# Optimization experiments

Measured on AMD Instinct MI355X. Metric: run time of the kernel, lower is better.

Reference implementation:

```python
import jax, jax.numpy as jnp
import numpy as np

B = 8192          # batch_size
NB = 4096         # num_banks (== mask length)
PAD = NB // 2     # reflect pad on each side


def setup_inputs() -> dict:
    key = jax.random.key(0)
    k1, k2, k3 = jax.random.split(key, 3)
    logits = jax.random.normal(k1, (NB,), dtype=jnp.float32) * 0.1
    u = jax.random.uniform(k2, (B, NB), dtype=jnp.float32)          # Bernoulli uniforms
    shift = jax.random.randint(k3, (B,), 0, NB, dtype=jnp.int32)    # per-sample shift
    return {"logits": logits, "u": u, "shift": shift}


def reference(logits, u, shift):
    # Bernoulli(sigmoid(logits)) sample via inverse-CDF on externally supplied uniforms
    p = jax.nn.sigmoid(logits)                       # (NB,)
    grid = (u < p).astype(jnp.float32)               # (B, NB)
    # Bernoulli log_prob summed over banks: g*log(p) + (1-g)*log(1-p)
    log_probs = (grid * jax.nn.log_sigmoid(logits)
                 + (1.0 - grid) * jax.nn.log_sigmoid(-logits)).sum(axis=1)  # (B,)
    # reflect-pad along bank axis, then gather a shifted window of length NB
    padded = jnp.pad(grid, ((0, 0), (PAD, PAD)), mode="reflect")    # (B, NB+2*PAD)
    idx = shift[:, None].astype(jnp.int32) + jnp.arange(NB, dtype=jnp.int32)[None, :]
    masks = jnp.take_along_axis(padded, idx, axis=1)[:, None, :]    # (B, 1, NB)
    return masks, log_probs
```

## Files before the change

### kernel.cpp

```cpp
#include <hip/hip_runtime.h>
#include <math.h>
#include <stdint.h>

#define NB 4096
#define PAD 2048
#define BLOCK 256
#define PBLOCK 256
#define NW (NB / 32)

__device__ __forceinline__ int mirror_idx(int i) {
    i = ::abs(i);
    return (i < NB) ? i : (2 * (NB - 1) - i);
}

__device__ __forceinline__ void lds_barrier() {
    asm volatile("s_waitcnt lgkmcnt(0)\n\ts_barrier" ::: "memory");
}

__global__ void fbmp_precompute(const float* __restrict__ logits, float* __restrict__ ws) {
    __shared__ float sred[PBLOCK / 64];
    float lsnsum = 0.0f;
    for (int j = threadIdx.x; j < NB; j += PBLOCK) {
        float x = logits[j];
        double xd = (double)x;
        float e = (float)exp(-xd);
        float p = 1.0f / (1.0f + e);
        float lsp = (float)(-log1p(exp(-xd)));
        float lsn = (float)(-log1p(exp(xd)));
        ws[j] = p;
        ws[NB + j] = lsp - lsn;
        lsnsum += lsn;
    }
    #pragma unroll
    for (int off = 32; off > 0; off >>= 1)
        lsnsum += __shfl_down(lsnsum, off, 64);
    const int lane = threadIdx.x & 63;
    const int wid  = threadIdx.x >> 6;
    if (lane == 0) sred[wid] = lsnsum;
    __syncthreads();
    if (threadIdx.x == 0) {
        float t = 0.0f;
        #pragma unroll
        for (int w = 0; w < PBLOCK / 64; ++w) t += sred[w];
        ws[2 * NB] = t;
    }
}

__global__ __launch_bounds__(BLOCK, 8) void fbmp_main(
    const float* __restrict__ u, const int* __restrict__ shift,
    const float* __restrict__ ws,
    float* __restrict__ masks, float* __restrict__ logp)
{
    __shared__ uint32_t sbits[NW + 2];
    __shared__ float sred[BLOCK / 64];

    const int b = blockIdx.x;
    const int t = threadIdx.x;
    const int lane = t & 63;
    const int w = t >> 6;

    const float4* __restrict__ u4 = (const float4*)(u + (size_t)b * NB);
    const float4* __restrict__ p4 = (const float4*)ws;
    const float4* __restrict__ d4 = (const float4*)(ws + NB);
    const int s = shift[b] - PAD;

    float acc = 0.0f;
    #pragma unroll
    for (int i = 0; i < 4; ++i) {
        const int f = i * BLOCK + t;
        float4 uv = u4[f];
        float4 pv = p4[f];
        float4 dv = d4[f];
        bool c0 = uv.x < pv.x;
        bool c1 = uv.y < pv.y;
        bool c2 = uv.z < pv.z;
        bool c3 = uv.w < pv.w;
        acc += (c0 ? dv.x : 0.0f) + (c1 ? dv.y : 0.0f)
             + (c2 ? dv.z : 0.0f) + (c3 ? dv.w : 0.0f);
        uint32_t n = (c0 ? 1u : 0u) | (c1 ? 2u : 0u) | (c2 ? 4u : 0u) | (c3 ? 8u : 0u);
        uint32_t v = n | (((uint32_t)__shfl_xor((int)n, 1, 64)) << 4);
        v |= ((uint32_t)__shfl_xor((int)v, 2, 64)) << 8;
        v |= ((uint32_t)__shfl_xor((int)v, 4, 64)) << 16;
        if ((t & 7) == 0) sbits[i * (BLOCK / 8) + (t >> 3)] = v;
    }

    #pragma unroll
    for (int off = 32; off > 0; off >>= 1)
        acc += __shfl_down(acc, off, 64);
    if (lane == 0) sred[w] = acc;

    lds_barrier();

    const uint64_t REV4 = 0xF7B3D591E6A2C480ull;
    float4* __restrict__ m4 = (float4*)(masks + (size_t)b * NB);
    #pragma unroll
    for (int i = 0; i < 4; ++i) {
        const int q = 4 * w + i;
        const int f = 256 * q + 4 * lane + s;
        float4 o;
        if (f >= -3 && f <= 4095 && (f < 0 || f > 4092)) {
            float* po = &o.x;
            #pragma unroll
            for (int e = 0; e < 4; ++e) {
                int j = mirror_idx(f + e);
                po[e] = (float)((sbits[j >> 5] >> (j & 31)) & 1u);
            }
        } else {
            int sb; bool rev;
            if (f >= 0 && f <= 4092)      { sb = f;        rev = false; }
            else if (f < 0)               { sb = -f - 3;   rev = true;  }
            else                          { sb = 8187 - f; rev = true;  }
            uint32_t w0 = sbits[sb >> 5];
            uint32_t w1 = sbits[(sb >> 5) + 1];
            uint32_t nib = (uint32_t)((((uint64_t)w1 << 32) | w0) >> (sb & 31)) & 0xFu;
            if (rev) nib = (uint32_t)(REV4 >> (nib << 2)) & 0xFu;
            o.x = (nib & 1u) ? 1.0f : 0.0f;
            o.y = (nib & 2u) ? 1.0f : 0.0f;
            o.z = (nib & 4u) ? 1.0f : 0.0f;
            o.w = (nib & 8u) ? 1.0f : 0.0f;
        }
        m4[q * 64 + lane] = o;
    }

    if (t == 0) {
        float tot = 0.0f;
        #pragma unroll
        for (int ww = 0; ww < BLOCK / 64; ++ww) tot += sred[ww];
        logp[b] = tot + ws[2 * NB];
    }
}

extern "C" void kernel_launch(void* const* d_in, const int* in_sizes, int n_in,
                              void* d_out, int out_size, void* d_ws, size_t ws_size,
                              hipStream_t stream) {
    const float* logits = (const float*)d_in[0];
    const float* u      = (const float*)d_in[1];
    const int*   shift  = (const int*)d_in[2];
    const int B = in_sizes[2];

    float* ws    = (float*)d_ws;
    float* masks = (float*)d_out;
    float* logp  = (float*)d_out + (size_t)B * NB;

    fbmp_precompute<<<1, PBLOCK, 0, stream>>>(logits, ws);
    fbmp_main<<<B, BLOCK, 0, stream>>>(u, shift, ws, masks, logp);
}
```

Measured before the change: 253.9 us.

## Process multiple rows per block with LDS-cached probabilities and prefetched uniforms

The main kernel now handles 8 rows per block. It caches p and delta in LDS once per block and software-prefetches the next row's uniforms while processing the current one, with double-buffered bit arrays. The precompute kernel is spread across 16 blocks that write partial sums, and the main kernel adds those partials together. This cuts the per-block launch and ws reload overhead and overlaps loads with compute. In exchange the grid shrinks to 1024 blocks, occupancy drops, and each block uses more registers and LDS.

New measurement: 249.7 us. About the same (-1.7%).

```diff
diff --git a/kernel.cpp b/kernel.cpp
--- a/kernel.cpp
+++ b/kernel.cpp
@@ -5,8 +5,9 @@
 #define NB 4096
 #define PAD 2048
 #define BLOCK 256
-#define PBLOCK 256
 #define NW (NB / 32)
+#define ROWS 8
+#define NPART 16
 
 __device__ __forceinline__ int mirror_idx(int i) {
     i = ::abs(i);
@@ -18,115 +19,144 @@
 }
 
 __global__ void fbmp_precompute(const float* __restrict__ logits, float* __restrict__ ws) {
-    __shared__ float sred[PBLOCK / 64];
-    float lsnsum = 0.0f;
-    for (int j = threadIdx.x; j < NB; j += PBLOCK) {
-        float x = logits[j];
-        double xd = (double)x;
-        float e = (float)exp(-xd);
-        float p = 1.0f / (1.0f + e);
-        float lsp = (float)(-log1p(exp(-xd)));
-        float lsn = (float)(-log1p(exp(xd)));
-        ws[j] = p;
-        ws[NB + j] = lsp - lsn;
-        lsnsum += lsn;
-    }
+    __shared__ float sred[BLOCK / 64];
+    const int j = blockIdx.x * BLOCK + threadIdx.x;
+    float x = logits[j];
+    double xd = (double)x;
+    float e = (float)exp(-xd);
+    float p = 1.0f / (1.0f + e);
+    float lsp = (float)(-log1p(exp(-xd)));
+    float lsn = (float)(-log1p(exp(xd)));
+    ws[j] = p;
+    ws[NB + j] = lsp - lsn;
+    float a = lsn;
     #pragma unroll
     for (int off = 32; off > 0; off >>= 1)
-        lsnsum += __shfl_down(lsnsum, off, 64);
-    const int lane = threadIdx.x & 63;
-    const int wid  = threadIdx.x >> 6;
-    if (lane == 0) sred[wid] = lsnsum;
+        a += __shfl_down(a, off, 64);
+    if ((threadIdx.x & 63) == 0) sred[threadIdx.x >> 6] = a;
     __syncthreads();
     if (threadIdx.x == 0) {
         float t = 0.0f;
         #pragma unroll
-        for (int w = 0; w < PBLOCK / 64; ++w) t += sred[w];
-        ws[2 * NB] = t;
+        for (int w = 0; w < BLOCK / 64; ++w) t += sred[w];
+        ws[2 * NB + blockIdx.x] = t;
     }
 }
 
-__global__ __launch_bounds__(BLOCK, 8) void fbmp_main(
+__global__ __launch_bounds__(BLOCK, 4) void fbmp_main(
     const float* __restrict__ u, const int* __restrict__ shift,
     const float* __restrict__ ws,
     float* __restrict__ masks, float* __restrict__ logp)
 {
-    __shared__ uint32_t sbits[NW + 2];
-    __shared__ float sred[BLOCK / 64];
+    __shared__ float s_p[NB];
+    __shared__ float s_d[NB];
+    __shared__ uint32_t sbits[2][NW + 2];
+    __shared__ float sred[ROWS][BLOCK / 64];
 
     const int b = blockIdx.x;
     const int t = threadIdx.x;
     const int lane = t & 63;
     const int w = t >> 6;
+    const int row0 = b * ROWS;
 
-    const float4* __restrict__ u4 = (const float4*)(u + (size_t)b * NB);
-    const float4* __restrict__ p4 = (const float4*)ws;
-    const float4* __restrict__ d4 = (const float4*)(ws + NB);
-    const int s = shift[b] - PAD;
+    float base = 0.0f;
+    #pragma unroll
+    for (int k = 0; k < NPART; ++k) base += ws[2 * NB + k];
 
-    float acc = 0.0f;
+    const float4* __restrict__ p4g = (const float4*)ws;
+    const float4* __restrict__ d4g = (const float4*)(ws + NB);
     #pragma unroll
-    for (int i = 0; i < 4; ++i) {
-        const int f = i * BLOCK + t;
-        float4 uv = u4[f];
-        float4 pv = p4[f];
-        float4 dv = d4[f];
-        bool c0 = uv.x < pv.x;
-        bool c1 = uv.y < pv.y;
-        bool c2 = uv.z < pv.z;
-        bool c3 = uv.w < pv.w;
-        acc += (c0 ? dv.x : 0.0f) + (c1 ? dv.y : 0.0f)
-             + (c2 ? dv.z : 0.0f) + (c3 ? dv.w : 0.0f);
-        uint32_t n = (c0 ? 1u : 0u) | (c1 ? 2u : 0u) | (c2 ? 4u : 0u) | (c3 ? 8u : 0u);
-        uint32_t v = n | (((uint32_t)__shfl_xor((int)n, 1, 64)) << 4);
-        v |= ((uint32_t)__shfl_xor((int)v, 2, 64)) << 8;
-        v |= ((uint32_t)__shfl_xor((int)v, 4, 64)) << 16;
-        if ((t & 7) == 0) sbits[i * (BLOCK / 8) + (t >> 3)] = v;
+    for (int i = 0; i < 4; ++i) ((float4*)s_p)[i * BLOCK + t] = p4g[i * BLOCK + t];
+    #pragma unroll
+    for (int i = 0; i < 4; ++i) ((float4*)s_d)[i * BLOCK + t] = d4g[i * BLOCK + t];
+
+    float4 ucur[4], unext[4];
+    {
+        const float4* __restrict__ u0 = (const float4*)(u + (size_t)row0 * NB);
+        #pragma unroll
+        for (int i = 0; i < 4; ++i) ucur[i] = u0[i * BLOCK + t];
     }
-
-    #pragma unroll
-    for (int off = 32; off > 0; off >>= 1)
-        acc += __shfl_down(acc, off, 64);
-    if (lane == 0) sred[w] = acc;
-
-    lds_barrier();
+    __syncthreads();
 
     const uint64_t REV4 = 0xF7B3D591E6A2C480ull;
-    float4* __restrict__ m4 = (float4*)(masks + (size_t)b * NB);
-    #pragma unroll
-    for (int i = 0; i < 4; ++i) {
-        const int q = 4 * w + i;
-        const int f = 256 * q + 4 * lane + s;
-        float4 o;
-        if (f >= -3 && f <= 4095 && (f < 0 || f > 4092)) {
-            float* po = &o.x;
+
+    for (int r = 0; r < ROWS; ++r) {
+        if (r + 1 < ROWS) {
+            const float4* __restrict__ un =
+                (const float4*)(u + (size_t)(row0 + r + 1) * NB);
             #pragma unroll
-            for (int e = 0; e < 4; ++e) {
-                int j = mirror_idx(f + e);
-                po[e] = (float)((sbits[j >> 5] >> (j & 31)) & 1u);
+            for (int i = 0; i < 4; ++i) unext[i] = un[i * BLOCK + t];
+        }
+        const int s = shift[row0 + r] - PAD;
+
+        uint32_t* __restrict__ sbw = sbits[r & 1];
+        float acc = 0.0f;
+        #pragma unroll
+        for (int i = 0; i < 4; ++i) {
+            float4 pv = ((const float4*)s_p)[i * BLOCK + t];
+            float4 dv = ((const float4*)s_d)[i * BLOCK + t];
+            bool c0 = ucur[i].x < pv.x;
+            bool c1 = ucur[i].y < pv.y;
+            bool c2 = ucur[i].z < pv.z;
+            bool c3 = ucur[i].w < pv.w;
+            acc += (c0 ? dv.x : 0.0f) + (c1 ? dv.y : 0.0f)
+                 + (c2 ? dv.z : 0.0f) + (c3 ? dv.w : 0.0f);
+            uint32_t n = (c0 ? 1u : 0u) | (c1 ? 2u : 0u) | (c2 ? 4u : 0u) | (c3 ? 8u : 0u);
+            uint32_t v = n | (((uint32_t)__shfl_xor((int)n, 1, 64)) << 4);
+            v |= ((uint32_t)__shfl_xor((int)v, 2, 64)) << 8;
+            v |= ((uint32_t)__shfl_xor((int)v, 4, 64)) << 16;
+            if ((t & 7) == 0) sbw[i * (BLOCK / 8) + (t >> 3)] = v;
+        }
+
+        #pragma unroll
+        for (int off = 32; off > 0; off >>= 1)
+            acc += __shfl_down(acc, off, 64);
+        if (lane == 0) sred[r][w] = acc;
+
+        lds_barrier();
+
+        float4* __restrict__ m4 = (float4*)(masks + (size_t)(row0 + r) * NB);
+        #pragma unroll
+        for (int i = 0; i < 4; ++i) {
+            const int q = 4 * w + i;
+            const int f = 256 * q + 4 * lane + s;
+            float4 o;
+            if (f >= -3 && f <= 4095 && (f < 0 || f > 4092)) {
+                float* po = &o.x;
+                #pragma unroll
+                for (int e = 0; e < 4; ++e) {
+                    int j = mirror_idx(f + e);
+                    po[e] = (float)((sbw[j >> 5] >> (j & 31)) & 1u);
+                }
+            } else {
+                int sb; bool rev;
+                if (f >= 0 && f <= 4092)      { sb = f;        rev = false; }
+                else if (f < 0)               { sb = -f - 3;   rev = true;  }
+                else                          { sb = 8187 - f; rev = true;  }
+                uint32_t w0 = sbw[sb >> 5];
+                uint32_t w1 = sbw[(sb >> 5) + 1];
+                uint32_t nib = (uint32_t)((((uint64_t)w1 << 32) | w0) >> (sb & 31)) & 0xFu;
+                if (rev) nib = (uint32_t)(REV4 >> (nib << 2)) & 0xFu;
+                o.x = (nib & 1u) ? 1.0f : 0.0f;
+                o.y = (nib & 2u) ? 1.0f : 0.0f;
+                o.z = (nib & 4u) ? 1.0f : 0.0f;
+                o.w = (nib & 8u) ? 1.0f : 0.0f;
             }
-        } else {
-            int sb; bool rev;
-            if (f >= 0 && f <= 4092)      { sb = f;        rev = false; }
-            else if (f < 0)               { sb = -f - 3;   rev = true;  }
-            else                          { sb = 8187 - f; rev = true;  }
-            uint32_t w0 = sbits[sb >> 5];
-            uint32_t w1 = sbits[(sb >> 5) + 1];
-            uint32_t nib = (uint32_t)((((uint64_t)w1 << 32) | w0) >> (sb & 31)) & 0xFu;
-            if (rev) nib = (uint32_t)(REV4 >> (nib << 2)) & 0xFu;
-            o.x = (nib & 1u) ? 1.0f : 0.0f;
-            o.y = (nib & 2u) ? 1.0f : 0.0f;
-            o.z = (nib & 4u) ? 1.0f : 0.0f;
-            o.w = (nib & 8u) ? 1.0f : 0.0f;
+            m4[q * 64 + lane] = o;
         }
-        m4[q * 64 + lane] = o;
+
+        #pragma unroll
+        for (int i = 0; i < 4; ++i) ucur[i] = unext[i];
     }
 
     if (t == 0) {
-        float tot = 0.0f;
         #pragma unroll
-        for (int ww = 0; ww < BLOCK / 64; ++ww) tot += sred[ww];
-        logp[b] = tot + ws[2 * NB];
+        for (int r = 0; r < ROWS; ++r) {
+            float tot = 0.0f;
+            #pragma unroll
+            for (int ww = 0; ww < BLOCK / 64; ++ww) tot += sred[r][ww];
+            logp[row0 + r] = tot + base;
+        }
     }
 }
 
@@ -142,6 +172,6 @@
     float* masks = (float*)d_out;
     float* logp  = (float*)d_out + (size_t)B * NB;
 
-    fbmp_precompute<<<1, PBLOCK, 0, stream>>>(logits, ws);
-    fbmp_main<<<B, BLOCK, 0, stream>>>(u, shift, ws, masks, logp);
+    fbmp_precompute<<<NPART, BLOCK, 0, stream>>>(logits, ws);
+    fbmp_main<<<B / ROWS, BLOCK, 0, stream>>>(u, shift, ws, masks, logp);
 }
```
